# Optimization experiments

Hardware: AMD Instinct MI355X
Metric: run time of the kernel (lower is better)

The kernel has to match this reference:

```python
import jax, jax.numpy as jnp
import numpy as np

NUM_HEADS = 8
NUM_POINTS = 4            # sampling points per pillar point
NUM_PILLAR = 4            # points in pillar
SAMPLING_RADIUS = 0.12


def masked_softmax(logits, mask):
    # logits/mask: [B, N, H, P]; softmax over last dim, robust to fully-masked rows
    m = mask.astype(logits.dtype)
    w = jax.nn.softmax(jnp.where(mask, logits, jnp.asarray(-1e9, logits.dtype)), axis=-1) * m
    return w / jnp.clip(jnp.sum(w, axis=-1, keepdims=True), 1e-6)


def grid_sample_bilinear(feat, loc):
    # feat: [G, D, H, W]; loc: [G, Nq, P, 2] normalized to [0,1]
    # matches torch grid_sample(mode='bilinear', padding_mode='zeros', align_corners=False)
    G, D, H, W = feat.shape
    _, Nq, P, _ = loc.shape
    fm = feat.reshape(G, D, H * W).transpose(0, 2, 1)  # [G, HW, D]
    x = loc[..., 0] * W - 0.5
    y = loc[..., 1] * H - 0.5
    x0 = jnp.floor(x)
    y0 = jnp.floor(y)
    wx = x - x0
    wy = y - y0
    out = jnp.zeros((G, Nq * P, D), dtype=feat.dtype)
    corners = [(0, 0, (1 - wx) * (1 - wy)), (1, 0, wx * (1 - wy)),
               (0, 1, (1 - wx) * wy), (1, 1, wx * wy)]
    for dx, dy, w in corners:
        xi = x0 + dx
        yi = y0 + dy
        valid = (xi >= 0) & (xi < W) & (yi >= 0) & (yi < H)
        xc = jnp.clip(xi, 0, W - 1).astype(jnp.int32)
        yc = jnp.clip(yi, 0, H - 1).astype(jnp.int32)
        idx = (yc * W + xc).reshape(G, Nq * P)
        g = jnp.take_along_axis(fm, idx[:, :, None], axis=1)  # [G, Nq*P, D]
        out = out + g * (w * valid.astype(feat.dtype)).reshape(G, Nq * P, 1)
    return out.reshape(G, Nq, P, D)


def setup_inputs() -> dict:
    key = jax.random.key(0)
    ks = jax.random.split(key, 10)
    B, N, C = 1, 10000, 256
    n_cams, Himg, Wimg = 6, 60, 100
    HD = NUM_HEADS * NUM_PILLAR * NUM_POINTS  # 128
    query = jax.random.normal(ks[0], (B, N, C), jnp.float32)
    image_feats = jax.random.normal(ks[1], (B, n_cams, C, Himg, Wimg), jnp.float32)
    reference_points_cam = jax.random.uniform(ks[2], (B, n_cams, N, NUM_PILLAR, 2), jnp.float32)
    bev_mask = jax.random.bernoulli(ks[3], 0.4, (B, n_cams, N, NUM_PILLAR))
    s = 0.02
    offset_W = jax.random.normal(ks[4], (C, HD * 2), jnp.float32) * s
    offset_b = jnp.zeros((HD * 2,), jnp.float32)
    weight_W = jax.random.normal(ks[5], (C, HD), jnp.float32) * s
    weight_b = jnp.zeros((HD,), jnp.float32)
    out_W = jax.random.normal(ks[6], (C, C), jnp.float32) * s
    out_b = jnp.zeros((C,), jnp.float32)
    return {"query": query, "image_feats": image_feats,
            "reference_points_cam": reference_points_cam, "bev_mask": bev_mask,
            "offset_W": offset_W, "offset_b": offset_b,
            "weight_W": weight_W, "weight_b": weight_b,
            "out_W": out_W, "out_b": out_b}


def reference(query, image_feats, reference_points_cam, bev_mask,
              offset_W, offset_b, weight_W, weight_b, out_W, out_b):
    B, N, C = query.shape
    _, n_cams, _, Himg, Wimg = image_feats.shape
    Hh, Pp, Pn = NUM_HEADS, NUM_PILLAR, NUM_POINTS
    P = Pp * Pn
    hd = C // Hh

    offsets = jnp.tanh(query @ offset_W + offset_b) * SAMPLING_RADIUS
    offsets = offsets.reshape(B, N, Hh, Pp, Pn, 2)
    weight_logits = (query @ weight_W + weight_b).reshape(B, N, Hh, P)

    fused = jnp.zeros((B, N, C), query.dtype)
    counts = jnp.zeros((B, N), jnp.int32)
    for cam in range(n_cams):
        ref = reference_points_cam[:, cam]          # [B, N, Pp, 2]
        visible = bev_mask[:, cam]                  # [B, N, Pp]
        loc = ref[:, :, None, :, None, :] + offsets  # [B, N, H, Pp, Pn, 2]
        loc = loc.reshape(B, N, Hh, P, 2)
        vmask = jnp.broadcast_to(visible[:, :, None, :, None], (B, N, Hh, Pp, Pn)).reshape(B, N, Hh, P)
        w = masked_softmax(weight_logits, vmask)    # [B, N, H, P]
        feat = image_feats[:, cam].reshape(B * Hh, hd, Himg, Wimg)
        grid = loc.transpose(0, 2, 1, 3, 4).reshape(B * Hh, N, P, 2)
        samp = grid_sample_bilinear(feat, grid)     # [B*H, N, P, hd]
        samp = samp.reshape(B, Hh, N, P, hd).transpose(0, 2, 1, 3, 4)  # [B, N, H, P, hd]
        cam_out = jnp.sum(samp * w[..., None], axis=3).reshape(B, N, C)
        has_vis = jnp.any(visible, axis=-1)         # [B, N]
        fused = fused + cam_out * has_vis[..., None].astype(cam_out.dtype)
        counts = counts + has_vis.astype(jnp.int32)
    fused = fused / jnp.clip(counts, 1)[..., None].astype(fused.dtype)
    return fused @ out_W + out_b
```

## Files before the change

kernel.cpp:

```cpp
#include <hip/hip_runtime.h>
#include <hip/hip_bf16.h>

#define N_Q   10000
#define N_CAM 6
#define HIMG  60
#define WIMG  100
#define NPIX  6000

typedef __attribute__((ext_vector_type(4))) float f32x4;
typedef __attribute__((ext_vector_type(8))) short bf16x8;

__device__ __forceinline__ unsigned short f2bf(float x) {
  __hip_bfloat16 b = __float2bfloat16(x);
  return *reinterpret_cast<unsigned short*>(&b);
}
__device__ __forceinline__ float bf2f(unsigned short u) {
  return __uint_as_float(((unsigned)u) << 16);
}
__device__ __forceinline__ float bf16lo(unsigned int u) {
  return __uint_as_float(u << 16);
}
__device__ __forceinline__ float bf16hi(unsigned int u) {
  return __uint_as_float(u & 0xffff0000u);
}

#define TRANS_BLKS (N_CAM * 94)

__global__ __launch_bounds__(256) void prep_trans_k(
    const float* __restrict__ in,
    const float* __restrict__ q,
    const float* __restrict__ oW, const float* __restrict__ wW,
    const float* __restrict__ outW,
    unsigned short* __restrict__ ftout,
    unsigned short* __restrict__ qh,    unsigned short* __restrict__ ql,
    unsigned short* __restrict__ oWth,  unsigned short* __restrict__ oWtl,
    unsigned short* __restrict__ wWth,  unsigned short* __restrict__ wWtl,
    unsigned short* __restrict__ outWth,unsigned short* __restrict__ outWtl) {
  __shared__ float tile[64][65];
  const int tid = threadIdx.x;
  if (blockIdx.x < TRANS_BLKS) {
    const int cam = blockIdx.x / 94;
    const int px0 = (blockIdx.x % 94) * 64;
    const int lpx = tid & 63;
    const int cg  = tid >> 6;
    const int px  = px0 + lpx;
    const bool pv = px < NPIX;

    for (int c0 = 0; c0 < 256; c0 += 64) {
#pragma unroll
      for (int i = 0; i < 16; ++i) {
        int cc = cg * 16 + i;
        tile[lpx][cc] = pv ? in[(cam * 256 + c0 + cc) * NPIX + px] : 0.f;
      }
      __syncthreads();
      const int wc = tid & 63;
      const int pg = tid >> 6;
#pragma unroll
      for (int i = 0; i < 16; ++i) {
        int lp = pg * 16 + i;
        int gpx = px0 + lp;
        if (gpx < NPIX)
          ftout[(size_t)(cam * NPIX + gpx) * 256 + c0 + wc] = f2bf(tile[lp][wc]);
      }
      __syncthreads();
    }
    return;
  }
  const int b = blockIdx.x - TRANS_BLKS;
  const int k = tid;
  float v; unsigned short *dh, *dl; int idx;
  if (b < N_Q) {
    v = q[b * 256 + k]; dh = qh; dl = ql; idx = b * 256 + k;
  } else if (b < N_Q + 256) {
    int nn = b - N_Q; v = oW[k * 256 + nn]; dh = oWth; dl = oWtl; idx = nn * 256 + k;
  } else if (b < N_Q + 384) {
    int nn = b - N_Q - 256; v = wW[k * 128 + nn]; dh = wWth; dl = wWtl; idx = nn * 256 + k;
  } else {
    int nn = b - N_Q - 384; v = outW[k * 256 + nn]; dh = outWth; dl = outWtl; idx = nn * 256 + k;
  }
  unsigned short hv = f2bf(v);
  dh[idx] = hv;
  dl[idx] = f2bf(v - bf2f(hv));
}

__device__ __forceinline__ void gemm_body(
    const unsigned short* __restrict__ Ah, const unsigned short* __restrict__ Al,
    const unsigned short* __restrict__ Bh, const unsigned short* __restrict__ Bl,
    const float* __restrict__ bias, float* __restrict__ C,
    int M, int N, int mode, int bm, int bn, int tid) {
  const int l = tid & 63, w = tid >> 6;
  const int wm = w >> 1, wn = w & 1;
  const int lr = l & 15;
  const int lk = (l >> 4) * 8;

  const int am0 = min(bm + wm * 32 + lr, M - 1);
  const int am1 = min(bm + wm * 32 + 16 + lr, M - 1);
  const int bn0 = bn + wn * 32 + lr;
  const int bn1 = bn0 + 16;

  const bf16x8* pah0 = (const bf16x8*)(Ah + (size_t)am0 * 256 + lk);
  const bf16x8* pah1 = (const bf16x8*)(Ah + (size_t)am1 * 256 + lk);
  const bf16x8* pal0 = (const bf16x8*)(Al + (size_t)am0 * 256 + lk);
  const bf16x8* pal1 = (const bf16x8*)(Al + (size_t)am1 * 256 + lk);
  const bf16x8* pbh0 = (const bf16x8*)(Bh + (size_t)bn0 * 256 + lk);
  const bf16x8* pbh1 = (const bf16x8*)(Bh + (size_t)bn1 * 256 + lk);
  const bf16x8* pbl0 = (const bf16x8*)(Bl + (size_t)bn0 * 256 + lk);
  const bf16x8* pbl1 = (const bf16x8*)(Bl + (size_t)bn1 * 256 + lk);

  f32x4 acc00 = {}, acc01 = {}, acc10 = {}, acc11 = {};

#pragma unroll
  for (int ks = 0; ks < 8; ++ks) {
    bf16x8 ah0 = pah0[ks * 4], ah1 = pah1[ks * 4];
    bf16x8 al0 = pal0[ks * 4], al1 = pal1[ks * 4];
    bf16x8 bh0 = pbh0[ks * 4], bh1 = pbh1[ks * 4];
    bf16x8 bl0 = pbl0[ks * 4], bl1 = pbl1[ks * 4];
    acc00 = __builtin_amdgcn_mfma_f32_16x16x32_bf16(ah0, bh0, acc00, 0, 0, 0);
    acc00 = __builtin_amdgcn_mfma_f32_16x16x32_bf16(ah0, bl0, acc00, 0, 0, 0);
    acc00 = __builtin_amdgcn_mfma_f32_16x16x32_bf16(al0, bh0, acc00, 0, 0, 0);
    acc01 = __builtin_amdgcn_mfma_f32_16x16x32_bf16(ah0, bh1, acc01, 0, 0, 0);
    acc01 = __builtin_amdgcn_mfma_f32_16x16x32_bf16(ah0, bl1, acc01, 0, 0, 0);
    acc01 = __builtin_amdgcn_mfma_f32_16x16x32_bf16(al0, bh1, acc01, 0, 0, 0);
    acc10 = __builtin_amdgcn_mfma_f32_16x16x32_bf16(ah1, bh0, acc10, 0, 0, 0);
    acc10 = __builtin_amdgcn_mfma_f32_16x16x32_bf16(ah1, bl0, acc10, 0, 0, 0);
    acc10 = __builtin_amdgcn_mfma_f32_16x16x32_bf16(al1, bh0, acc10, 0, 0, 0);
    acc11 = __builtin_amdgcn_mfma_f32_16x16x32_bf16(ah1, bh1, acc11, 0, 0, 0);
    acc11 = __builtin_amdgcn_mfma_f32_16x16x32_bf16(ah1, bl1, acc11, 0, 0, 0);
    acc11 = __builtin_amdgcn_mfma_f32_16x16x32_bf16(al1, bh1, acc11, 0, 0, 0);
  }

  const float bias0 = bias[bn + wn * 32 + lr];
  const float bias1 = bias[bn + wn * 32 + 16 + lr];
  const int row0 = bm + wm * 32 + (l >> 4) * 4;
  const int col0 = bn + wn * 32 + lr;
#pragma unroll
  for (int r = 0; r < 4; ++r) {
    int rowA = row0 + r, rowB = row0 + 16 + r;
    float v00 = acc00[r] + bias0, v01 = acc01[r] + bias1;
    float v10 = acc10[r] + bias0, v11 = acc11[r] + bias1;
    if (mode == 1) {
      v00 = tanhf(v00) * 0.12f; v01 = tanhf(v01) * 0.12f;
      v10 = tanhf(v10) * 0.12f; v11 = tanhf(v11) * 0.12f;
    }
    if (rowA < M) {
      C[(size_t)rowA * N + col0] = v00;
      C[(size_t)rowA * N + col0 + 16] = v01;
    }
    if (rowB < M) {
      C[(size_t)rowB * N + col0] = v10;
      C[(size_t)rowB * N + col0 + 16] = v11;
    }
  }
}

__global__ __launch_bounds__(256) void gemm12_k(
    const unsigned short* __restrict__ Ah, const unsigned short* __restrict__ Al,
    const unsigned short* __restrict__ B1h, const unsigned short* __restrict__ B1l,
    const float* __restrict__ b1, float* __restrict__ C1,
    const unsigned short* __restrict__ B2h, const unsigned short* __restrict__ B2l,
    const float* __restrict__ b2, float* __restrict__ C2) {
  const int by = blockIdx.y;
  if (by < 4)
    gemm_body(Ah, Al, B1h, B1l, b1, C1, N_Q, 256, 1,
              blockIdx.x * 64, by * 64, threadIdx.x);
  else
    gemm_body(Ah, Al, B2h, B2l, b2, C2, N_Q, 128, 0,
              blockIdx.x * 64, (by - 4) * 64, threadIdx.x);
}

__global__ __launch_bounds__(256) void gemm_out_k(
    const unsigned short* __restrict__ Ah, const unsigned short* __restrict__ Al,
    const unsigned short* __restrict__ Bh, const unsigned short* __restrict__ Bl,
    const float* __restrict__ bias, float* __restrict__ C) {
  gemm_body(Ah, Al, Bh, Bl, bias, C, N_Q, 256, 0,
            blockIdx.x * 64, blockIdx.y * 64, threadIdx.x);
}

__global__ __launch_bounds__(256) void sample_cam(
    const unsigned short* __restrict__ ft,
    const float* __restrict__ offs,
    const float* __restrict__ wlog,
    const float* __restrict__ refp,
    const int*   __restrict__ mask,
    float* __restrict__ partial) {
  const int tid = threadIdx.x;
  const int sub = tid >> 7;
  const int t   = tid & 127;
  const int cam = blockIdx.x / (N_Q / 2);
  const int n   = (blockIdx.x % (N_Q / 2)) * 2 + sub;
  const int h   = t >> 4;
  const int p   = t & 15;
  const int pp  = p >> 2;
  const int c   = (t >> 2) & 3;
  const int ch  = t & 3;

  const int vis = mask[(cam * N_Q + n) * 4 + pp];
  const unsigned long long bal = __ballot(vis != 0);
  if (!(bal & 0x1111ULL)) return;

  __shared__ float spt[2][1216];
  float* lds = spt[sub];
  unsigned int* ldsu = reinterpret_cast<unsigned int*>(lds);

  const float2 off = reinterpret_cast<const float2*>(offs)[n * 128 + t];
  const float logit = wlog[n * 128 + t];
  const uint4* ftq = reinterpret_cast<const uint4*>(ft);

  const int abase = h * 152 + p * 9;
  const int rbase = h * 152;
  const unsigned gbase = (unsigned)(h * 4 + ch);

  float val = vis ? logit : -1e30f;
#pragma unroll
  for (int m = 8; m >= 1; m >>= 1)
    val = fmaxf(val, __shfl_xor(val, m, 16));
  float e = vis ? __expf(logit - val) : 0.f;
  float s = e;
#pragma unroll
  for (int m = 8; m >= 1; m >>= 1)
    s += __shfl_xor(s, m, 16);
  const float wgt = e / fmaxf(s, 1e-6f);

  const float2 ref = reinterpret_cast<const float2*>(refp)[(cam * N_Q + n) * 4 + pp];
  const float x = fmaf(ref.x + off.x, (float)WIMG, -0.5f);
  const float y = fmaf(ref.y + off.y, (float)HIMG, -0.5f);
  const float x0f = floorf(x), y0f = floorf(y);
  const float wx = x - x0f, wy = y - y0f;
  const int x0 = (int)x0f, y0 = (int)y0f;
  const int x1 = x0 + 1, y1 = y0 + 1;
  const float mx0 = (x0 >= 0 && x0 < WIMG) ? 1.f : 0.f;
  const float mx1 = (x1 >= 0 && x1 < WIMG) ? 1.f : 0.f;
  const float my0 = (y0 >= 0 && y0 < HIMG) ? 1.f : 0.f;
  const float my1 = (y1 >= 0 && y1 < HIMG) ? 1.f : 0.f;
  const int xc0 = min(max(x0, 0), WIMG - 1);
  const int xc1 = min(max(x1, 0), WIMG - 1);
  const int yc0 = min(max(y0, 0), HIMG - 1);
  const int yc1 = min(max(y1, 0), HIMG - 1);
  lds[abase + 0] = (1.f - wx) * (1.f - wy) * mx0 * my0 * wgt;
  lds[abase + 1] = wx * (1.f - wy) * mx1 * my0 * wgt;
  lds[abase + 2] = (1.f - wx) * wy * mx0 * my1 * wgt;
  lds[abase + 3] = wx * wy * mx1 * my1 * wgt;
  ldsu[abase + 4] = (unsigned)(yc0 * WIMG + xc0);
  ldsu[abase + 5] = (unsigned)(yc0 * WIMG + xc1);
  ldsu[abase + 6] = (unsigned)(yc1 * WIMG + xc0);
  ldsu[abase + 7] = (unsigned)(yc1 * WIMG + xc1);
  __builtin_amdgcn_wave_barrier();

  float acc[8] = {0.f, 0.f, 0.f, 0.f, 0.f, 0.f, 0.f, 0.f};
  const unsigned camq = (unsigned)cam * (NPIX * 32);
  const bool pv0 = (bal      ) & 1ULL;
  const bool pv1 = (bal >>  4) & 1ULL;
  const bool pv2 = (bal >>  8) & 1ULL;
  const bool pv3 = (bal >> 12) & 1ULL;
  uint4 u0[4], u1[4], u2[4], u3[4];

#define ISSUE(U, P)                                                          \
  if (pv##P) {                                                               \
    _Pragma("unroll")                                                        \
    for (int pn = 0; pn < 4; ++pn) {                                         \
      const unsigned pix = ldsu[rbase + ((P) * 4 + pn) * 9 + 4 + c];         \
      U[pn] = ftq[camq + pix * 32u + gbase];                                 \
    }                                                                        \
  }
  ISSUE(u0, 0) ISSUE(u1, 1) ISSUE(u2, 2) ISSUE(u3, 3)

#define CONSUME(U, P)                                                        \
  if (pv##P) {                                                               \
    _Pragma("unroll")                                                        \
    for (int pn = 0; pn < 4; ++pn) {                                         \
      const float wv = lds[rbase + ((P) * 4 + pn) * 9 + c];                  \
      acc[0] = fmaf(bf16lo(U[pn].x), wv, acc[0]);                            \
      acc[1] = fmaf(bf16hi(U[pn].x), wv, acc[1]);                            \
      acc[2] = fmaf(bf16lo(U[pn].y), wv, acc[2]);                            \
      acc[3] = fmaf(bf16hi(U[pn].y), wv, acc[3]);                            \
      acc[4] = fmaf(bf16lo(U[pn].z), wv, acc[4]);                            \
      acc[5] = fmaf(bf16hi(U[pn].z), wv, acc[5]);                            \
      acc[6] = fmaf(bf16lo(U[pn].w), wv, acc[6]);                            \
      acc[7] = fmaf(bf16hi(U[pn].w), wv, acc[7]);                            \
    }                                                                        \
  }
  CONSUME(u0, 0) CONSUME(u1, 1) CONSUME(u2, 2) CONSUME(u3, 3)
#undef ISSUE
#undef CONSUME

#pragma unroll
  for (int j = 0; j < 8; ++j) acc[j] += __shfl_xor(acc[j], 4);
#pragma unroll
  for (int j = 0; j < 8; ++j) acc[j] += __shfl_xor(acc[j], 8);

  if (c == 0) {
    float* pb = partial + ((size_t)cam * N_Q + n) * 256 + h * 32 + ch * 8;
    f32x4 a0 = {acc[0], acc[1], acc[2], acc[3]};
    f32x4 a1 = {acc[4], acc[5], acc[6], acc[7]};
    *reinterpret_cast<f32x4*>(pb)     = a0;
    *reinterpret_cast<f32x4*>(pb + 4) = a1;
  }
}

__global__ __launch_bounds__(256) void combine_k(
    const float* __restrict__ partial,
    const int*   __restrict__ mask,
    unsigned short* __restrict__ fh,
    unsigned short* __restrict__ fl) {
  const int tid = threadIdx.x;
  const int sub = tid >> 7;
  const int t   = tid & 127;
  const int n   = blockIdx.x * 2 + sub;

  __shared__ int sv[2][6];
  if (t < 6) {
    const int4 m4 = *reinterpret_cast<const int4*>(&mask[(t * N_Q + n) * 4]);
    sv[sub][t] = (m4.x | m4.y | m4.z | m4.w) ? 1 : 0;
  }
  __syncthreads();

  float sx = 0.f, sy = 0.f;
  int cnt = 0;
#pragma unroll
  for (int cam = 0; cam < N_CAM; ++cam) {
    if (sv[sub][cam]) {
      const float2 v =
          reinterpret_cast<const float2*>(partial)[((size_t)cam * N_Q + n) * 128 + t];
      sx += v.x; sy += v.y; cnt++;
    }
  }
  const float inv = (cnt > 0) ? (1.f / (float)cnt) : 1.f;
  const float v0 = sx * inv, v1 = sy * inv;
  const unsigned short h0 = f2bf(v0), h1 = f2bf(v1);
  const unsigned short l0 = f2bf(v0 - bf2f(h0)), l1 = f2bf(v1 - bf2f(h1));
  reinterpret_cast<unsigned int*>(fh)[n * 128 + t] = (unsigned)h0 | ((unsigned)h1 << 16);
  reinterpret_cast<unsigned int*>(fl)[n * 128 + t] = (unsigned)l0 | ((unsigned)l1 << 16);
}

extern "C" void kernel_launch(void* const* d_in, const int* in_sizes, int n_in,
                              void* d_out, int out_size, void* d_ws, size_t ws_size,
                              hipStream_t stream) {
  const float* query = (const float*)d_in[0];
  const float* feats = (const float*)d_in[1];
  const float* refp  = (const float*)d_in[2];
  const int*   mask  = (const int*)d_in[3];
  const float* oW    = (const float*)d_in[4];
  const float* ob    = (const float*)d_in[5];
  const float* wW    = (const float*)d_in[6];
  const float* wb    = (const float*)d_in[7];
  const float* outW  = (const float*)d_in[8];
  const float* outb  = (const float*)d_in[9];
  float* out = (float*)d_out;

  char* wsb = (char*)d_ws;
  size_t o = 0;
  unsigned short* ft = (unsigned short*)(wsb + o); o += (size_t)N_CAM * NPIX * 256 * 2;
  unsigned short* qh = (unsigned short*)(wsb + o); o += (size_t)N_Q * 256 * 2;
  unsigned short* ql = (unsigned short*)(wsb + o); o += (size_t)N_Q * 256 * 2;
  unsigned short* fh = (unsigned short*)(wsb + o); o += (size_t)N_Q * 256 * 2;
  unsigned short* fl = (unsigned short*)(wsb + o); o += (size_t)N_Q * 256 * 2;
  unsigned short* oWth  = (unsigned short*)(wsb + o); o += 256 * 256 * 2;
  unsigned short* oWtl  = (unsigned short*)(wsb + o); o += 256 * 256 * 2;
  unsigned short* wWth  = (unsigned short*)(wsb + o); o += 128 * 256 * 2;
  unsigned short* wWtl  = (unsigned short*)(wsb + o); o += 128 * 256 * 2;
  unsigned short* outWth = (unsigned short*)(wsb + o); o += 256 * 256 * 2;
  unsigned short* outWtl = (unsigned short*)(wsb + o); o += 256 * 256 * 2;
  float* offs    = (float*)(wsb + o); o += (size_t)N_Q * 256 * 4;
  float* wlog    = (float*)(wsb + o); o += (size_t)N_Q * 128 * 4;
  float* partial = (float*)(wsb + o); o += (size_t)N_CAM * N_Q * 256 * 4;

  prep_trans_k<<<TRANS_BLKS + N_Q + 640, 256, 0, stream>>>(
      feats, query, oW, wW, outW, ft, qh, ql,
      oWth, oWtl, wWth, wWtl, outWth, outWtl);

  dim3 g12((N_Q + 63) / 64, 6);
  gemm12_k<<<g12, 256, 0, stream>>>(qh, ql, oWth, oWtl, ob, offs,
                                    wWth, wWtl, wb, wlog);

  sample_cam<<<N_CAM * (N_Q / 2), 256, 0, stream>>>(ft, offs, wlog, refp, mask,
                                                    partial);

  combine_k<<<N_Q / 2, 256, 0, stream>>>(partial, mask, fh, fl);

  dim3 g3((N_Q + 63) / 64, 4);
  gemm_out_k<<<g3, 256, 0, stream>>>(fh, fl, outWth, outWtl, outb, out);
}
```

Measured before the change: 170.2 us.

## Fuse exp into weight GEMM, use packed FMA, swap GEMM grid order

The weight-logit GEMM epilogue now applies exp directly, so the sampling kernel drops the per-head max reduction and its exp. Without the max subtraction, large logits could overflow in exp. The bilinear accumulation uses v_pk_fma_f32 via inline asm to halve the FMA instruction count. The GEMM grids are transposed so blocks that share the same A row-tile run next to each other, which should improve L2 reuse of the activation tiles.

```diff
diff --git a/kernel.cpp b/kernel.cpp
--- a/kernel.cpp
+++ b/kernel.cpp
@@ -8,6 +8,7 @@
 #define NPIX  6000
 
 typedef __attribute__((ext_vector_type(4))) float f32x4;
+typedef __attribute__((ext_vector_type(2))) float f32x2;
 typedef __attribute__((ext_vector_type(8))) short bf16x8;
 
 __device__ __forceinline__ unsigned short f2bf(float x) {
@@ -22,6 +23,9 @@
 }
 __device__ __forceinline__ float bf16hi(unsigned int u) {
   return __uint_as_float(u & 0xffff0000u);
+}
+__device__ __forceinline__ void pk_fma(f32x2& acc, f32x2 a, f32x2 b) {
+  asm("v_pk_fma_f32 %0, %1, %2, %0" : "+v"(acc) : "v"(a), "v"(b));
 }
 
 #define TRANS_BLKS (N_CAM * 94)
@@ -141,6 +145,9 @@
     if (mode == 1) {
       v00 = tanhf(v00) * 0.12f; v01 = tanhf(v01) * 0.12f;
       v10 = tanhf(v10) * 0.12f; v11 = tanhf(v11) * 0.12f;
+    } else if (mode == 2) {
+      v00 = __expf(v00); v01 = __expf(v01);
+      v10 = __expf(v10); v11 = __expf(v11);
     }
     if (rowA < M) {
       C[(size_t)rowA * N + col0] = v00;
@@ -159,13 +166,13 @@
     const float* __restrict__ b1, float* __restrict__ C1,
     const unsigned short* __restrict__ B2h, const unsigned short* __restrict__ B2l,
     const float* __restrict__ b2, float* __restrict__ C2) {
-  const int by = blockIdx.y;
+  const int by = blockIdx.x;
   if (by < 4)
     gemm_body(Ah, Al, B1h, B1l, b1, C1, N_Q, 256, 1,
-              blockIdx.x * 64, by * 64, threadIdx.x);
+              blockIdx.y * 64, by * 64, threadIdx.x);
   else
-    gemm_body(Ah, Al, B2h, B2l, b2, C2, N_Q, 128, 0,
-              blockIdx.x * 64, (by - 4) * 64, threadIdx.x);
+    gemm_body(Ah, Al, B2h, B2l, b2, C2, N_Q, 128, 2,
+              blockIdx.y * 64, (by - 4) * 64, threadIdx.x);
 }
 
 __global__ __launch_bounds__(256) void gemm_out_k(
@@ -173,7 +180,7 @@
     const unsigned short* __restrict__ Bh, const unsigned short* __restrict__ Bl,
     const float* __restrict__ bias, float* __restrict__ C) {
   gemm_body(Ah, Al, Bh, Bl, bias, C, N_Q, 256, 0,
-            blockIdx.x * 64, blockIdx.y * 64, threadIdx.x);
+            blockIdx.y * 64, blockIdx.x * 64, threadIdx.x);
 }
 
 __global__ __launch_bounds__(256) void sample_cam(
@@ -203,18 +210,14 @@
   unsigned int* ldsu = reinterpret_cast<unsigned int*>(lds);
 
   const float2 off = reinterpret_cast<const float2*>(offs)[n * 128 + t];
-  const float logit = wlog[n * 128 + t];
+  const float E = wlog[n * 128 + t];
   const uint4* ftq = reinterpret_cast<const uint4*>(ft);
 
   const int abase = h * 152 + p * 9;
   const int rbase = h * 152;
   const unsigned gbase = (unsigned)(h * 4 + ch);
 
-  float val = vis ? logit : -1e30f;
-#pragma unroll
-  for (int m = 8; m >= 1; m >>= 1)
-    val = fmaxf(val, __shfl_xor(val, m, 16));
-  float e = vis ? __expf(logit - val) : 0.f;
+  float e = vis ? E : 0.f;
   float s = e;
 #pragma unroll
   for (int m = 8; m >= 1; m >>= 1)
@@ -246,7 +249,7 @@
   ldsu[abase + 7] = (unsigned)(yc1 * WIMG + xc1);
   __builtin_amdgcn_wave_barrier();
 
-  float acc[8] = {0.f, 0.f, 0.f, 0.f, 0.f, 0.f, 0.f, 0.f};
+  f32x2 acc2[4] = {{0.f, 0.f}, {0.f, 0.f}, {0.f, 0.f}, {0.f, 0.f}};
   const unsigned camq = (unsigned)cam * (NPIX * 32);
   const bool pv0 = (bal      ) & 1ULL;
   const bool pv1 = (bal >>  4) & 1ULL;
@@ -269,20 +272,21 @@
     _Pragma("unroll")                                                        \
     for (int pn = 0; pn < 4; ++pn) {                                         \
       const float wv = lds[rbase + ((P) * 4 + pn) * 9 + c];                  \
-      acc[0] = fmaf(bf16lo(U[pn].x), wv, acc[0]);                            \
-      acc[1] = fmaf(bf16hi(U[pn].x), wv, acc[1]);                            \
-      acc[2] = fmaf(bf16lo(U[pn].y), wv, acc[2]);                            \
-      acc[3] = fmaf(bf16hi(U[pn].y), wv, acc[3]);                            \
-      acc[4] = fmaf(bf16lo(U[pn].z), wv, acc[4]);                            \
-      acc[5] = fmaf(bf16hi(U[pn].z), wv, acc[5]);                            \
-      acc[6] = fmaf(bf16lo(U[pn].w), wv, acc[6]);                            \
-      acc[7] = fmaf(bf16hi(U[pn].w), wv, acc[7]);                            \
+      const f32x2 w2 = {wv, wv};                                             \
+      f32x2 a;                                                               \
+      a.x = bf16lo(U[pn].x); a.y = bf16hi(U[pn].x); pk_fma(acc2[0], a, w2);  \
+      a.x = bf16lo(U[pn].y); a.y = bf16hi(U[pn].y); pk_fma(acc2[1], a, w2);  \
+      a.x = bf16lo(U[pn].z); a.y = bf16hi(U[pn].z); pk_fma(acc2[2], a, w2);  \
+      a.x = bf16lo(U[pn].w); a.y = bf16hi(U[pn].w); pk_fma(acc2[3], a, w2);  \
     }                                                                        \
   }
   CONSUME(u0, 0) CONSUME(u1, 1) CONSUME(u2, 2) CONSUME(u3, 3)
 #undef ISSUE
 #undef CONSUME
 
+  float acc[8];
+#pragma unroll
+  for (int j = 0; j < 4; ++j) { acc[2 * j] = acc2[j].x; acc[2 * j + 1] = acc2[j].y; }
 #pragma unroll
   for (int j = 0; j < 8; ++j) acc[j] += __shfl_xor(acc[j], 4);
 #pragma unroll
@@ -368,7 +372,7 @@
       feats, query, oW, wW, outW, ft, qh, ql,
       oWth, oWtl, wWth, wWtl, outWth, outWtl);
 
-  dim3 g12((N_Q + 63) / 64, 6);
+  dim3 g12(6, (N_Q + 63) / 64);
   gemm12_k<<<g12, 256, 0, stream>>>(qh, ql, oWth, oWtl, ob, offs,
                                     wWth, wWtl, wb, wlog);
 
@@ -377,6 +381,6 @@
 
   combine_k<<<N_Q / 2, 256, 0, stream>>>(partial, mask, fh, fl);
 
-  dim3 g3((N_Q + 63) / 64, 4);
+  dim3 g3(4, (N_Q + 63) / 64);
   gemm_out_k<<<g3, 256, 0, stream>>>(fh, fl, outWth, outWtl, outb, out);
 }
```

After: 170.2 us. About the same (-0.0%).
